# Optimization experiments

Hardware: AMD Instinct MI355X
Metric: run time of the kernel (lower is better)

The kernel has to match this reference:

```python
import jax, jax.numpy as jnp
import numpy as np

T, B, I, H, L = 512, 32, 256, 512, 3  # seq_len, batch, input_size, hidden_size, num_layers


def setup_inputs() -> dict:
    key = jax.random.key(0)
    ks = jax.random.split(key, 2 + 2 * L)
    d = {}
    d["x"] = jax.random.normal(ks[0], (T, B, I), dtype=jnp.float32)
    d["h0"] = jax.random.normal(ks[1], (2 * L, B, H), dtype=jnp.float32)
    in_dims = [I, 2 * H, 2 * H]
    for l in range(L):
        k_ih, k_hh = jax.random.split(ks[2 + l], 2)
        d[f"w_ih{l}"] = jax.random.normal(k_ih, (2, in_dims[l], 3 * H), dtype=jnp.float32) * np.float32(1.0 / np.sqrt(in_dims[l]))
        d[f"w_hh{l}"] = jax.random.normal(k_hh, (2, H, 3 * H), dtype=jnp.float32) * np.float32(1.0 / np.sqrt(H))
        d[f"b_ih{l}"] = jnp.zeros((2, 3 * H), dtype=jnp.float32)
        d[f"b_hh{l}"] = jnp.zeros((2, 3 * H), dtype=jnp.float32)
    return d


def _gru_direction(xs, h0d, w_ih, w_hh, b_ih, b_hh, reverse):
    # xs: (T, B, in_dim). Precompute all input-side gates in one big GEMM.
    gi = jnp.einsum('tbi,ig->tbg', xs, w_ih) + b_ih  # (T, B, 3H)

    def step(h, g):
        gh = h @ w_hh + b_hh                         # (B, 3H)
        i_r, i_z, i_n = jnp.split(g, 3, axis=-1)
        h_r, h_z, h_n = jnp.split(gh, 3, axis=-1)
        r = jax.nn.sigmoid(i_r + h_r)
        z = jax.nn.sigmoid(i_z + h_z)
        n = jnp.tanh(i_n + r * h_n)
        h_new = (1.0 - z) * n + z * h
        return h_new, h_new

    _, ys = jax.lax.scan(step, h0d, gi, reverse=reverse)
    return ys  # (T, B, H), aligned with input time order


def reference(x, h0, w_ih0, w_hh0, b_ih0, b_hh0,
              w_ih1, w_hh1, b_ih1, b_hh1,
              w_ih2, w_hh2, b_ih2, b_hh2):
    params = [(w_ih0, w_hh0, b_ih0, b_hh0),
              (w_ih1, w_hh1, b_ih1, b_hh1),
              (w_ih2, w_hh2, b_ih2, b_hh2)]
    layer_in = x
    for l, (w_ih, w_hh, b_ih, b_hh) in enumerate(params):
        fwd = _gru_direction(layer_in, h0[2 * l], w_ih[0], w_hh[0], b_ih[0], b_hh[0], reverse=False)
        bwd = _gru_direction(layer_in, h0[2 * l + 1], w_ih[1], w_hh[1], b_ih[1], b_hh[1], reverse=True)
        layer_in = jnp.concatenate([fwd, bwd], axis=-1)  # (T, B, 2H)
    return layer_in
```

## Files before the change

kernel.cpp:

```cpp
#include <hip/hip_runtime.h>

#define T_LEN 512
#define BATCH 32
#define HSZ 512
#define G3 1536

typedef unsigned int u32;
typedef unsigned long long u64;
typedef unsigned short u16;
typedef __attribute__((ext_vector_type(8))) short bf16x8;
typedef __attribute__((ext_vector_type(4))) float f32x4;

static __device__ __forceinline__ u16 f2bf(float x) {
  u32 u = __float_as_uint(x);
  u32 r = (u + 0x7FFFu + ((u >> 16) & 1u)) >> 16;
  return (u16)r;
}
static __device__ __forceinline__ u32 pack_bf16(float a, float b) {
  return (u32)f2bf(a) | ((u32)f2bf(b) << 16);
}
static __device__ __forceinline__ float nz(float x) { return (x == x) ? x : 0.f; }

__global__ __launch_bounds__(256) void transpose_bf16(
    const float* __restrict__ src, u16* __restrict__ dst, int K, int N)
{
  int dirz = blockIdx.z;
  src += (size_t)dirz * K * N;
  dst += (size_t)dirz * N * K;
  __shared__ float tile[32][33];
  int n0 = blockIdx.x * 32, k0 = blockIdx.y * 32;
  int tx = threadIdx.x & 31, ty = threadIdx.x >> 5;
#pragma unroll
  for (int i = ty; i < 32; i += 8)
    tile[i][tx] = src[(size_t)(k0 + i) * N + n0 + tx];
  __syncthreads();
#pragma unroll
  for (int i = ty; i < 32; i += 8)
    dst[(size_t)(n0 + i) * K + k0 + tx] = f2bf(tile[tx][i]);
}

__global__ __launch_bounds__(256) void convert_x(
    const float* __restrict__ src, u16* __restrict__ dst, int n4)
{
  int i = blockIdx.x * 256 + threadIdx.x;
  if (i >= n4) return;
  float4 v = ((const float4*)src)[i];
  union { u16 h[4]; uint2 u; } o;
  o.h[0] = f2bf(v.x); o.h[1] = f2bf(v.y); o.h[2] = f2bf(v.z); o.h[3] = f2bf(v.w);
  ((uint2*)dst)[i] = o.u;
}

__global__ __launch_bounds__(256) void gemm_gi(
    const u16* __restrict__ A,
    const u16* __restrict__ Bw,
    const float* __restrict__ bias,
    _Float16* __restrict__ C,
    int M, int K)
{
  const int N = G3;
  int dir = blockIdx.z;
  const u16* Bd = Bw + (size_t)dir * N * K;
  _Float16* Cd = C + (size_t)dir * M * N;
  const float* biasd = bias + dir * N;

  int tm = blockIdx.x * 128;
  int tn = blockIdx.y * 128;

  __shared__ u16 sA[128][40];
  __shared__ u16 sB[128][40];

  int tid = threadIdx.x;
  int lane = tid & 63, wave = tid >> 6;
  int wm = (wave & 1) << 6, wn = (wave >> 1) << 6;

  f32x4 acc[4][4] = {};

  int srow = tid >> 1, shalf = (tid & 1) << 4;
  const u16* pa = A + (size_t)(tm + srow) * K + shalf;
  const u16* pb = Bd + (size_t)(tn + srow) * K + shalf;

  for (int k0 = 0; k0 < K; k0 += 32) {
    uint4 va0 = *(const uint4*)(pa + k0);
    uint4 va1 = *(const uint4*)(pa + k0 + 8);
    uint4 vb0 = *(const uint4*)(pb + k0);
    uint4 vb1 = *(const uint4*)(pb + k0 + 8);
    *(uint4*)&sA[srow][shalf]     = va0;
    *(uint4*)&sA[srow][shalf + 8] = va1;
    *(uint4*)&sB[srow][shalf]     = vb0;
    *(uint4*)&sB[srow][shalf + 8] = vb1;
    __syncthreads();
    int kg = (lane >> 4) << 3;
    int r16 = lane & 15;
    bf16x8 af[4], bfr[4];
#pragma unroll
    for (int f = 0; f < 4; f++) {
      af[f]  = *(const bf16x8*)&sA[wm + f * 16 + r16][kg];
      bfr[f] = *(const bf16x8*)&sB[wn + f * 16 + r16][kg];
    }
#pragma unroll
    for (int fm = 0; fm < 4; fm++)
#pragma unroll
      for (int fn = 0; fn < 4; fn++)
        acc[fm][fn] = __builtin_amdgcn_mfma_f32_16x16x32_bf16(af[fm], bfr[fn], acc[fm][fn], 0, 0, 0);
    __syncthreads();
  }

  int col4 = lane & 15, rbase = (lane >> 4) << 2;
#pragma unroll
  for (int fn = 0; fn < 4; fn++) {
    int col = tn + wn + fn * 16 + col4;
    float bv = biasd[col];
#pragma unroll
    for (int fm = 0; fm < 4; fm++) {
      int row0 = tm + wm + fm * 16 + rbase;
#pragma unroll
      for (int r = 0; r < 4; r++)
        Cd[(size_t)(row0 + r) * N + col] = (_Float16)nz(acc[fm][fn][r] + bv);
    }
  }
}

__global__ __launch_bounds__(64, 1) void gru_rec(
    const _Float16* __restrict__ gi,
    const u16* __restrict__ whhT,
    const float* __restrict__ bhh,
    const float* __restrict__ h0,
    float* __restrict__ outF,
    u16* __restrict__ outB,
    u32* __restrict__ hbuf,
    int* __restrict__ flags,
    int base)
{
  int dir = blockIdx.x >> 5;
  int jc  = blockIdx.x & 31;
  int lane = threadIdx.x;
  int l15 = lane & 15;
  int q   = lane >> 4;
  int j   = jc * 16 + l15;
  int kq  = q * 8;

  __shared__ u16 sW[3][16][520];

  for (int idx = lane; idx < 48 * 64; idx += 64) {
    int row = idx >> 6, c = idx & 63;
    int g = row >> 4, jl = row & 15;
    const u16* src = whhT + ((size_t)dir * G3 + g * 512 + jc * 16 + jl) * HSZ + c * 8;
    *(uint4*)&sW[g][jl][c * 8] = *(const uint4*)src;
  }
  __syncthreads();

  float bhr = bhh[dir * G3 + j];
  float bhz = bhh[dir * G3 + 512 + j];
  float bhn = bhh[dir * G3 + 1024 + j];

  float hm[8];
#pragma unroll
  for (int mt = 0; mt < 2; mt++)
#pragma unroll
    for (int r = 0; r < 4; r++)
      hm[mt * 4 + r] = h0[((size_t)dir * BATCH + mt * 16 + q * 4 + r) * HSZ + j];

  {
    u32* hb = hbuf + (size_t)dir * (BATCH * HSZ / 2);
#pragma unroll
    for (int i = 0; i < 8; i++) {
      int b = (i >> 2) * 16 + q * 4 + (i & 3);
      float partner = __shfl_xor(hm[i], 1);
      if (!(l15 & 1))
        __hip_atomic_store(&hb[(size_t)b * (HSZ / 2) + (j >> 1)], pack_bf16(hm[i], partner),
                           __ATOMIC_RELAXED, __HIP_MEMORY_SCOPE_AGENT);
    }
  }
  __builtin_amdgcn_fence(__ATOMIC_RELEASE, "workgroup");
  __builtin_amdgcn_s_waitcnt(0);
  if (lane == 0)
    __hip_atomic_store(&flags[(dir * 32 + jc) * 16], base + 1,
                       __ATOMIC_RELAXED, __HIP_MEMORY_SCOPE_AGENT);

  for (int t = 0; t < T_LEN; t++) {
    int t_eff = dir ? (T_LEN - 1 - t) : t;

    const _Float16* gib = gi + (((size_t)dir * T_LEN + t_eff) * BATCH) * G3;
    float gv[3][8];
#pragma unroll
    for (int g = 0; g < 3; g++)
#pragma unroll
      for (int i = 0; i < 8; i++) {
        int b = (i >> 2) * 16 + q * 4 + (i & 3);
        gv[g][i] = (float)gib[(size_t)b * G3 + g * 512 + j];
      }

    {
      int target = base + t + 1;
      const int* fl = &flags[(dir * 32 + (lane & 31)) * 16];
      while (true) {
        int f = __hip_atomic_load(fl, __ATOMIC_RELAXED, __HIP_MEMORY_SCOPE_AGENT);
        if (__ballot(f >= target) == ~0ull) break;
        __builtin_amdgcn_s_sleep(1);
      }
      __builtin_amdgcn_fence(__ATOMIC_ACQUIRE, "workgroup");
    }

    const u32* hc = hbuf + ((size_t)(t & 1) * 2 + dir) * (BATCH * HSZ / 2);
    union { u64 q[2]; bf16x8 v; } a0[16], a1[16];
#pragma unroll
    for (int kg = 0; kg < 16; kg++) {
      const u32* p0 = hc + (size_t)l15 * (HSZ / 2) + kg * 16 + (kq >> 1);
      const u32* p1 = hc + (size_t)(16 + l15) * (HSZ / 2) + kg * 16 + (kq >> 1);
      a0[kg].q[0] = __hip_atomic_load((const u64*)p0,       __ATOMIC_RELAXED, __HIP_MEMORY_SCOPE_AGENT);
      a0[kg].q[1] = __hip_atomic_load((const u64*)(p0 + 2), __ATOMIC_RELAXED, __HIP_MEMORY_SCOPE_AGENT);
      a1[kg].q[0] = __hip_atomic_load((const u64*)p1,       __ATOMIC_RELAXED, __HIP_MEMORY_SCOPE_AGENT);
      a1[kg].q[1] = __hip_atomic_load((const u64*)(p1 + 2), __ATOMIC_RELAXED, __HIP_MEMORY_SCOPE_AGENT);
    }

    f32x4 aR0 = {}, aR1 = {}, aZ0 = {}, aZ1 = {}, aN0 = {}, aN1 = {};
#pragma unroll
    for (int kg = 0; kg < 16; kg++) {
      bf16x8 wR = *(const bf16x8*)&sW[0][l15][kg * 32 + kq];
      bf16x8 wZ = *(const bf16x8*)&sW[1][l15][kg * 32 + kq];
      bf16x8 wN = *(const bf16x8*)&sW[2][l15][kg * 32 + kq];
      aR0 = __builtin_amdgcn_mfma_f32_16x16x32_bf16(a0[kg].v, wR, aR0, 0, 0, 0);
      aR1 = __builtin_amdgcn_mfma_f32_16x16x32_bf16(a1[kg].v, wR, aR1, 0, 0, 0);
      aZ0 = __builtin_amdgcn_mfma_f32_16x16x32_bf16(a0[kg].v, wZ, aZ0, 0, 0, 0);
      aZ1 = __builtin_amdgcn_mfma_f32_16x16x32_bf16(a1[kg].v, wZ, aZ1, 0, 0, 0);
      aN0 = __builtin_amdgcn_mfma_f32_16x16x32_bf16(a0[kg].v, wN, aN0, 0, 0, 0);
      aN1 = __builtin_amdgcn_mfma_f32_16x16x32_bf16(a1[kg].v, wN, aN1, 0, 0, 0);
    }

    float hv[8];
#pragma unroll
    for (int mt = 0; mt < 2; mt++)
#pragma unroll
      for (int r = 0; r < 4; r++) {
        int i = mt * 4 + r;
        float aR = mt ? aR1[r] : aR0[r];
        float aZ = mt ? aZ1[r] : aZ0[r];
        float aN = mt ? aN1[r] : aN0[r];
        float xr = gv[0][i] + aR + bhr;
        float xz = gv[1][i] + aZ + bhz;
        xr = fminf(fmaxf(xr, -40.f), 40.f);
        xz = fminf(fmaxf(xz, -40.f), 40.f);
        float rr = 1.f / (1.f + __expf(-xr));
        float zz = 1.f / (1.f + __expf(-xz));
        float xn = gv[2][i] + rr * (aN + bhn);
        xn = fminf(fmaxf(xn, -15.f), 15.f);
        float e2 = __expf(2.f * xn);
        float nn = (e2 - 1.f) / (e2 + 1.f);
        hv[i] = (1.f - zz) * nn + zz * hm[i];
        hm[i] = hv[i];
      }

    u32* hn = hbuf + ((size_t)((t + 1) & 1) * 2 + dir) * (BATCH * HSZ / 2);
#pragma unroll
    for (int i = 0; i < 8; i++) {
      int b = (i >> 2) * 16 + q * 4 + (i & 3);
      float partner = __shfl_xor(hv[i], 1);
      if (!(l15 & 1))
        __hip_atomic_store(&hn[(size_t)b * (HSZ / 2) + (j >> 1)], pack_bf16(hv[i], partner),
                           __ATOMIC_RELAXED, __HIP_MEMORY_SCOPE_AGENT);
    }
    __builtin_amdgcn_fence(__ATOMIC_RELEASE, "workgroup");
    __builtin_amdgcn_s_waitcnt(0);
    if (lane == 0)
      __hip_atomic_store(&flags[(dir * 32 + jc) * 16], base + t + 2,
                         __ATOMIC_RELAXED, __HIP_MEMORY_SCOPE_AGENT);

#pragma unroll
    for (int i = 0; i < 8; i++) {
      int b = (i >> 2) * 16 + q * 4 + (i & 3);
      size_t oidx = ((size_t)t_eff * BATCH + b) * 1024 + dir * HSZ + j;
      if (outF) __builtin_nontemporal_store(hv[i], &outF[oidx]);
      if (outB) __builtin_nontemporal_store(f2bf(hv[i]), &outB[oidx]);
    }
  }
}

extern "C" void kernel_launch(void* const* d_in, const int* in_sizes, int n_in,
                              void* d_out, int out_size, void* d_ws, size_t ws_size,
                              hipStream_t stream)
{
  const float* x  = (const float*)d_in[0];
  const float* h0 = (const float*)d_in[1];
  const float* w_ih[3] = {(const float*)d_in[2], (const float*)d_in[6], (const float*)d_in[10]};
  const float* w_hh[3] = {(const float*)d_in[3], (const float*)d_in[7], (const float*)d_in[11]};
  const float* b_ih[3] = {(const float*)d_in[4], (const float*)d_in[8], (const float*)d_in[12]};
  const float* b_hh[3] = {(const float*)d_in[5], (const float*)d_in[9], (const float*)d_in[13]};

  char* ws = (char*)d_ws;
  size_t off = 0;
  auto alloc = [&](size_t bytes) {
    void* p = ws + off;
    off = (off + bytes + 255) & ~(size_t)255;
    return p;
  };
  int* flags = (int*)alloc(4096);
  u32* hbuf = (u32*)alloc((size_t)2 * 2 * BATCH * (HSZ / 2) * 4);
  u16* xbf  = (u16*)alloc((size_t)16384 * 256 * 2);
  u16* lobf = (u16*)alloc((size_t)16384 * 1024 * 2);
  u16* wihT[3];
  wihT[0] = (u16*)alloc((size_t)2 * G3 * 256 * 2);
  wihT[1] = (u16*)alloc((size_t)2 * G3 * 1024 * 2);
  wihT[2] = (u16*)alloc((size_t)2 * G3 * 1024 * 2);
  u16* whhT[3];
  for (int l = 0; l < 3; l++) whhT[l] = (u16*)alloc((size_t)2 * G3 * 512 * 2);
  _Float16* gi = (_Float16*)alloc((size_t)2 * T_LEN * BATCH * G3 * 2);

  hipMemsetAsync(flags, 0, 4096, stream);

  convert_x<<<4096, 256, 0, stream>>>(x, xbf, 16384 * 256 / 4);
  transpose_bf16<<<dim3(48, 8, 2),  256, 0, stream>>>(w_ih[0], wihT[0], 256,  G3);
  transpose_bf16<<<dim3(48, 32, 2), 256, 0, stream>>>(w_ih[1], wihT[1], 1024, G3);
  transpose_bf16<<<dim3(48, 32, 2), 256, 0, stream>>>(w_ih[2], wihT[2], 1024, G3);
  for (int l = 0; l < 3; l++)
    transpose_bf16<<<dim3(48, 16, 2), 256, 0, stream>>>(w_hh[l], whhT[l], 512, G3);

  const int M = T_LEN * BATCH;
  for (int l = 0; l < 3; l++) {
    int K = (l == 0) ? 256 : 1024;
    const u16* Ain = (l == 0) ? xbf : lobf;
    gemm_gi<<<dim3(M / 128, G3 / 128, 2), 256, 0, stream>>>(Ain, wihT[l], b_ih[l], gi, M, K);
    float* oF = (l == 2) ? (float*)d_out : nullptr;
    u16* oB = (l < 2) ? lobf : nullptr;
    gru_rec<<<64, 64, 0, stream>>>(gi, whhT[l], b_hh[l],
                                   h0 + (size_t)l * 2 * BATCH * HSZ,
                                   oF, oB, hbuf, flags, l * 513);
  }
}
```

Before: 7.332 ms.

## Transpose gi layout, hold recurrent weights in registers, use fast reciprocals

The input-gate GEMM now writes its output transposed (gate-column major, time*batch contiguous), so the recurrent kernel fetches each gate's batch values with two 8-byte vector loads per gate instead of scattered half-precision loads. The recurrent weights move from LDS into a per-lane register array of 48 bf16x8 fragments, removing LDS reads from the serial step loop but greatly increasing register pressure. Sigmoid and tanh divisions are replaced with the hardware approximate reciprocal, and the output stores drop the nontemporal hint. The register-resident weights may spill, and the approximate reciprocal slightly changes numerics.

```diff
diff --git a/kernel.cpp b/kernel.cpp
--- a/kernel.cpp
+++ b/kernel.cpp
@@ -4,6 +4,7 @@
 #define BATCH 32
 #define HSZ 512
 #define G3 1536
+#define MROWS 16384
 
 typedef unsigned int u32;
 typedef unsigned long long u64;
@@ -60,7 +61,7 @@
   const int N = G3;
   int dir = blockIdx.z;
   const u16* Bd = Bw + (size_t)dir * N * K;
-  _Float16* Cd = C + (size_t)dir * M * N;
+  _Float16* Cd = C + (size_t)dir * N * M;
   const float* biasd = bias + dir * N;
 
   int tm = blockIdx.x * 128;
@@ -113,9 +114,11 @@
 #pragma unroll
     for (int fm = 0; fm < 4; fm++) {
       int row0 = tm + wm + fm * 16 + rbase;
+      union { _Float16 h[4]; uint2 u; } o;
 #pragma unroll
       for (int r = 0; r < 4; r++)
-        Cd[(size_t)(row0 + r) * N + col] = (_Float16)nz(acc[fm][fn][r] + bv);
+        o.h[r] = (_Float16)nz(acc[fm][fn][r] + bv);
+      *(uint2*)&Cd[(size_t)col * M + row0] = o.u;
     }
   }
 }
@@ -139,15 +142,15 @@
   int j   = jc * 16 + l15;
   int kq  = q * 8;
 
-  __shared__ u16 sW[3][16][520];
-
-  for (int idx = lane; idx < 48 * 64; idx += 64) {
-    int row = idx >> 6, c = idx & 63;
-    int g = row >> 4, jl = row & 15;
-    const u16* src = whhT + ((size_t)dir * G3 + g * 512 + jc * 16 + jl) * HSZ + c * 8;
-    *(uint4*)&sW[g][jl][c * 8] = *(const uint4*)src;
-  }
-  __syncthreads();
+  bf16x8 wf[3][16];
+  {
+    const u16* wb = whhT + ((size_t)dir * G3 + j) * HSZ + kq;
+#pragma unroll
+    for (int g = 0; g < 3; g++)
+#pragma unroll
+      for (int kg = 0; kg < 16; kg++)
+        wf[g][kg] = *(const bf16x8*)(wb + ((size_t)g * 512) * HSZ + kg * 32);
+  }
 
   float bhr = bhh[dir * G3 + j];
   float bhz = bhh[dir * G3 + 512 + j];
@@ -180,15 +183,19 @@
   for (int t = 0; t < T_LEN; t++) {
     int t_eff = dir ? (T_LEN - 1 - t) : t;
 
-    const _Float16* gib = gi + (((size_t)dir * T_LEN + t_eff) * BATCH) * G3;
     float gv[3][8];
 #pragma unroll
-    for (int g = 0; g < 3; g++)
-#pragma unroll
-      for (int i = 0; i < 8; i++) {
-        int b = (i >> 2) * 16 + q * 4 + (i & 3);
-        gv[g][i] = (float)gib[(size_t)b * G3 + g * 512 + j];
+    for (int g = 0; g < 3; g++) {
+      const _Float16* gb = gi + ((size_t)dir * G3 + g * 512 + j) * MROWS + (size_t)t_eff * BATCH;
+      union { uint2 u; _Float16 h[4]; } v0, v1;
+      v0.u = *(const uint2*)(gb + q * 4);
+      v1.u = *(const uint2*)(gb + 16 + q * 4);
+#pragma unroll
+      for (int r = 0; r < 4; r++) {
+        gv[g][r]     = (float)v0.h[r];
+        gv[g][4 + r] = (float)v1.h[r];
       }
+    }
 
     {
       int target = base + t + 1;
@@ -216,15 +223,12 @@
     f32x4 aR0 = {}, aR1 = {}, aZ0 = {}, aZ1 = {}, aN0 = {}, aN1 = {};
 #pragma unroll
     for (int kg = 0; kg < 16; kg++) {
-      bf16x8 wR = *(const bf16x8*)&sW[0][l15][kg * 32 + kq];
-      bf16x8 wZ = *(const bf16x8*)&sW[1][l15][kg * 32 + kq];
-      bf16x8 wN = *(const bf16x8*)&sW[2][l15][kg * 32 + kq];
-      aR0 = __builtin_amdgcn_mfma_f32_16x16x32_bf16(a0[kg].v, wR, aR0, 0, 0, 0);
-      aR1 = __builtin_amdgcn_mfma_f32_16x16x32_bf16(a1[kg].v, wR, aR1, 0, 0, 0);
-      aZ0 = __builtin_amdgcn_mfma_f32_16x16x32_bf16(a0[kg].v, wZ, aZ0, 0, 0, 0);
-      aZ1 = __builtin_amdgcn_mfma_f32_16x16x32_bf16(a1[kg].v, wZ, aZ1, 0, 0, 0);
-      aN0 = __builtin_amdgcn_mfma_f32_16x16x32_bf16(a0[kg].v, wN, aN0, 0, 0, 0);
-      aN1 = __builtin_amdgcn_mfma_f32_16x16x32_bf16(a1[kg].v, wN, aN1, 0, 0, 0);
+      aR0 = __builtin_amdgcn_mfma_f32_16x16x32_bf16(a0[kg].v, wf[0][kg], aR0, 0, 0, 0);
+      aR1 = __builtin_amdgcn_mfma_f32_16x16x32_bf16(a1[kg].v, wf[0][kg], aR1, 0, 0, 0);
+      aZ0 = __builtin_amdgcn_mfma_f32_16x16x32_bf16(a0[kg].v, wf[1][kg], aZ0, 0, 0, 0);
+      aZ1 = __builtin_amdgcn_mfma_f32_16x16x32_bf16(a1[kg].v, wf[1][kg], aZ1, 0, 0, 0);
+      aN0 = __builtin_amdgcn_mfma_f32_16x16x32_bf16(a0[kg].v, wf[2][kg], aN0, 0, 0, 0);
+      aN1 = __builtin_amdgcn_mfma_f32_16x16x32_bf16(a1[kg].v, wf[2][kg], aN1, 0, 0, 0);
     }
 
     float hv[8];
@@ -240,12 +244,12 @@
         float xz = gv[1][i] + aZ + bhz;
         xr = fminf(fmaxf(xr, -40.f), 40.f);
         xz = fminf(fmaxf(xz, -40.f), 40.f);
-        float rr = 1.f / (1.f + __expf(-xr));
-        float zz = 1.f / (1.f + __expf(-xz));
+        float rr = __builtin_amdgcn_rcpf(1.f + __expf(-xr));
+        float zz = __builtin_amdgcn_rcpf(1.f + __expf(-xz));
         float xn = gv[2][i] + rr * (aN + bhn);
         xn = fminf(fmaxf(xn, -15.f), 15.f);
         float e2 = __expf(2.f * xn);
-        float nn = (e2 - 1.f) / (e2 + 1.f);
+        float nn = (e2 - 1.f) * __builtin_amdgcn_rcpf(e2 + 1.f);
         hv[i] = (1.f - zz) * nn + zz * hm[i];
         hm[i] = hv[i];
       }
@@ -269,8 +273,8 @@
     for (int i = 0; i < 8; i++) {
       int b = (i >> 2) * 16 + q * 4 + (i & 3);
       size_t oidx = ((size_t)t_eff * BATCH + b) * 1024 + dir * HSZ + j;
-      if (outF) __builtin_nontemporal_store(hv[i], &outF[oidx]);
-      if (outB) __builtin_nontemporal_store(f2bf(hv[i]), &outB[oidx]);
+      if (outF) outF[oidx] = hv[i];
+      if (outB) outB[oidx] = f2bf(hv[i]);
     }
   }
 }
```

New measurement: 9.459 ms. 29.0% more time.
